# Optimization experiments

Measured on AMD Instinct MI355X. Metric: run time of the kernel, lower is better.

Reference implementation:

```python
import jax, jax.numpy as jnp
import numpy as np

D = 1024
H = 16
HD = D // H
EPS = 1e-9


def setup_inputs() -> dict:
    key = jax.random.key(0)
    ks = jax.random.split(key, 16)
    B, Lq, Lk = 8, 512, 1024
    s = 0.02
    return {
        "q": jax.random.normal(ks[0], (B, Lq, D), jnp.float32),
        "q_mask": jnp.ones((B, Lq), jnp.bool_),
        "kv": jax.random.normal(ks[1], (B, Lk, D), jnp.float32),
        "kv_mask": jnp.ones((B, Lk), jnp.bool_),
        # MultiheadAttention packed in-proj + out-proj
        "in_proj_w": jax.random.normal(ks[2], (3 * D, D), jnp.float32) * s,
        "in_proj_b": jnp.zeros((3 * D,), jnp.float32),
        "out_w": jax.random.normal(ks[3], (D, D), jnp.float32) * s,
        "out_b": jnp.zeros((D,), jnp.float32),
        # shared LayerNorm
        "ln_g": jnp.ones((D,), jnp.float32),
        "ln_b": jnp.zeros((D,), jnp.float32),
        # FFN
        "w1": jax.random.normal(ks[4], (4 * D, D), jnp.float32) * s,
        "b1": jnp.zeros((4 * D,), jnp.float32),
        "w2": jax.random.normal(ks[5], (D, 4 * D), jnp.float32) * s,
        "b2": jnp.zeros((D,), jnp.float32),
        # gate MLP
        "gw1": jax.random.normal(ks[6], (D, 2 * D), jnp.float32) * s,
        "gb1": jnp.zeros((D,), jnp.float32),
        "gw2": jax.random.normal(ks[7], (1, D), jnp.float32) * s,
        "gb2": jnp.zeros((1,), jnp.float32),
    }


def _layer_norm(x, g, b, eps=1e-5):
    mu = x.mean(-1, keepdims=True)
    var = ((x - mu) ** 2).mean(-1, keepdims=True)
    return (x - mu) * jax.lax.rsqrt(var + eps) * g + b


def reference(q, q_mask, kv, kv_mask, in_proj_w, in_proj_b, out_w, out_b,
              ln_g, ln_b, w1, b1, w2, b2, gw1, gb1, gw2, gb2):
    B, Lq, _ = q.shape
    Lk = kv.shape[1]
    # packed projections (torch Linear convention: x @ W.T + b)
    qp = (q @ in_proj_w[:D].T + in_proj_b[:D]).reshape(B, Lq, H, HD)
    kp = (kv @ in_proj_w[D:2 * D].T + in_proj_b[D:2 * D]).reshape(B, Lk, H, HD)
    vp = (kv @ in_proj_w[2 * D:].T + in_proj_b[2 * D:]).reshape(B, Lk, H, HD)
    scores = jnp.einsum('bqhd,bkhd->bhqk', qp, kp) / np.sqrt(HD)  # (B,H,Lq,Lk)
    scores = jnp.where(kv_mask[:, None, None, :], scores, -1e30)
    attn = jax.nn.softmax(scores, axis=-1)
    ctx = jnp.einsum('bhqk,bkhd->bqhd', attn, vp).reshape(B, Lq, D)
    attn_out = ctx @ out_w.T + out_b
    # entropy over keys, normalized by log(Lk), averaged over heads
    p = jnp.clip(attn, EPS)
    ent = -(p * jnp.log(p)).sum(-1) / jnp.log(jnp.float32(Lk))  # (B,H,Lq)
    ent = ent.mean(axis=1)[..., None]  # (B,Lq,1)
    conf = jnp.clip(1.0 - ent, 0.0, 1.0)
    # gate MLP on [q, attn_out]
    h = jax.nn.gelu(jnp.concatenate([q, attn_out], -1) @ gw1.T + gb1, approximate=False)
    g = jax.nn.sigmoid(h @ gw2.T + gb2) * conf
    q2 = _layer_norm(q + attn_out * g, ln_g, ln_b)
    ffn = jax.nn.gelu(q2 @ w1.T + b1, approximate=False) @ w2.T + b2
    q2 = _layer_norm(q2 + ffn, ln_g, ln_b)
    return q2, ent
```

## Files before the change

### kernel.cpp

```cpp
#include <hip/hip_runtime.h>
#include <cstdint>
#include <cstddef>

typedef __bf16 bf16;
typedef __bf16 bf16x8 __attribute__((ext_vector_type(8)));
typedef __bf16 bf16x4 __attribute__((ext_vector_type(4)));
typedef float  f32x4  __attribute__((ext_vector_type(4)));

#define GLOAD_LDS16(g, l) __builtin_amdgcn_global_load_lds( \
    (const __attribute__((address_space(1))) unsigned int*)(g), \
    (__attribute__((address_space(3))) unsigned int*)(l), 16, 0, 0)

static constexpr int D_  = 1024;
static constexpr int H_  = 16;
static constexpr int HD_ = 64;
static constexpr int B_  = 8;
static constexpr int LQ_ = 512;
static constexpr int LK_ = 1024;
static constexpr int MQ_ = B_ * LQ_;
static constexpr float LOG2E_ = 1.4426950408889634f;
static constexpr float INV_LN_LK_ = 0.14426950408889634f;
static constexpr float CSHIFT_ = 8.0f;

__device__ __forceinline__ float gelu_f(float v) {
    return 0.5f * v * (1.0f + erff(v * 0.70710678118654752f));
}

__global__ __launch_bounds__(256)
void cast_all_k(const float* __restrict__ ipw, const float* __restrict__ outw,
                const float* __restrict__ w1,  const float* __restrict__ w2,
                const float* __restrict__ gw1, const float* __restrict__ q,
                const float* __restrict__ kv,
                bf16* __restrict__ ipw_b, bf16* __restrict__ outw_b,
                bf16* __restrict__ w1_b,  bf16* __restrict__ w2_b,
                bf16* __restrict__ gw1_b, bf16* __restrict__ x_b,
                bf16* __restrict__ kv_b) {
    const int b = blockIdx.x, t = threadIdx.x;
    const float* src; bf16* dst; long e;
    if (b < 1536)       { src = ipw;  dst = ipw_b;  e = (long)b * 2048; }
    else if (b < 2048)  { src = outw; dst = outw_b; e = (long)(b - 1536) * 2048; }
    else if (b < 4096)  { src = w1;   dst = w1_b;   e = (long)(b - 2048) * 2048; }
    else if (b < 6144)  { src = w2;   dst = w2_b;   e = (long)(b - 4096) * 2048; }
    else if (b < 7168)  { src = gw1;  dst = gw1_b;  e = (long)(b - 6144) * 2048; }
    else if (b < 11264) { src = kv;   dst = kv_b;   e = (long)(b - 7168) * 2048; }
    else {
        long e2 = (long)(b - 11264) * 2048 + t * 8;
        float4 a = *(const float4*)(q + e2);
        float4 c = *(const float4*)(q + e2 + 4);
        bf16x8 o;
        o[0]=(bf16)a.x; o[1]=(bf16)a.y; o[2]=(bf16)a.z; o[3]=(bf16)a.w;
        o[4]=(bf16)c.x; o[5]=(bf16)c.y; o[6]=(bf16)c.z; o[7]=(bf16)c.w;
        long row = e2 >> 10, col = e2 & 1023;
        *(bf16x8*)(x_b + row * 2048 + col) = o;
        return;
    }
    e += t * 8;
    float4 a = *(const float4*)(src + e);
    float4 c = *(const float4*)(src + e + 4);
    bf16x8 o;
    o[0]=(bf16)a.x; o[1]=(bf16)a.y; o[2]=(bf16)a.z; o[3]=(bf16)a.w;
    o[4]=(bf16)c.x; o[5]=(bf16)c.y; o[6]=(bf16)c.z; o[7]=(bf16)c.w;
    *(bf16x8*)(dst + e) = o;
}

template<int ACT>
__device__ __forceinline__
void gemm256_body(const bf16* __restrict__ A, int lda,
                  const bf16* __restrict__ W, int ldw,
                  const float* __restrict__ bias,
                  bf16* __restrict__ Cb, int ldcb, int K) {
    __shared__ __attribute__((aligned(16))) bf16 As[2][256 * 64];
    __shared__ __attribute__((aligned(16))) bf16 Bs[2][256 * 64];
    const int gx = gridDim.x;
    const int nwg = gx * gridDim.y;
    const int flat = blockIdx.x + gx * blockIdx.y;
    const int swzb = (flat & 7) * (nwg >> 3) + (flat >> 3);
    const int by = swzb / gx, bx = swzb - by * gx;
    const int t = threadIdx.x;
    const int w = t >> 6, l = t & 63, l15 = l & 15, lg = l >> 4;
    const int wr = w >> 2, wc = w & 3;
    const int row0 = by * 256, col0 = bx * 256;
    const int sw = l15 & 7;

    size_t aoff[4], woff[4];
    int ldsoff[4];
#pragma unroll
    for (int j = 0; j < 4; ++j) {
        int id = j * 512 + t;
        int r = id >> 3, c = id & 7;
        aoff[j] = (size_t)(row0 + r) * lda + ((c ^ (r & 7)) << 3);
        woff[j] = (size_t)(col0 + r) * ldw + ((c ^ (r & 7)) << 3);
        ldsoff[j] = (j * 512 + w * 64) * 8;
    }

    f32x4 acc[8][4];
#pragma unroll
    for (int m = 0; m < 8; ++m)
#pragma unroll
        for (int n = 0; n < 4; ++n) acc[m][n] = f32x4{0.f, 0.f, 0.f, 0.f};

    const int nt = K >> 6;
#pragma unroll
    for (int j = 0; j < 4; ++j) {
        GLOAD_LDS16(A + aoff[j], (bf16*)As[0] + ldsoff[j]);
        GLOAD_LDS16(W + woff[j], (bf16*)Bs[0] + ldsoff[j]);
    }
    __syncthreads();

    for (int kt = 0; kt < nt; ++kt) {
        const int cur = kt & 1;
        if (kt + 1 < nt) {
            const size_t k0 = (size_t)(kt + 1) * 64;
            bf16* dA = (bf16*)As[cur ^ 1];
            bf16* dB = (bf16*)Bs[cur ^ 1];
#pragma unroll
            for (int j = 0; j < 4; ++j) {
                GLOAD_LDS16(A + aoff[j] + k0, dA + ldsoff[j]);
                GLOAD_LDS16(W + woff[j] + k0, dB + ldsoff[j]);
            }
        }
        const bf16* Ac = As[cur];
        const bf16* Bc = Bs[cur];
#pragma unroll
        for (int ks2 = 0; ks2 < 2; ++ks2) {
            bf16x8 af[8], bfr[4];
#pragma unroll
            for (int m = 0; m < 8; ++m) {
                int ra = wr * 128 + m * 16 + l15;
                af[m] = *(const bf16x8*)&Ac[ra * 64 + (((ks2 * 4 + lg) ^ sw) << 3)];
            }
#pragma unroll
            for (int n = 0; n < 4; ++n) {
                int rb = wc * 64 + n * 16 + l15;
                bfr[n] = *(const bf16x8*)&Bc[rb * 64 + (((ks2 * 4 + lg) ^ sw) << 3)];
            }
#pragma unroll
            for (int m = 0; m < 8; ++m)
#pragma unroll
                for (int n = 0; n < 4; ++n)
                    acc[m][n] = __builtin_amdgcn_mfma_f32_16x16x32_bf16(af[m], bfr[n], acc[m][n], 0, 0, 0);
        }
        __syncthreads();
    }

#pragma unroll
    for (int n = 0; n < 4; ++n) {
        int gcol = col0 + wc * 64 + n * 16 + l15;
        float bv = bias[gcol];
#pragma unroll
        for (int m = 0; m < 8; ++m) {
            int grow = row0 + wr * 128 + m * 16 + lg * 4;
#pragma unroll
            for (int r = 0; r < 4; ++r) {
                float v = acc[m][n][r] + bv;
                if (ACT) v = gelu_f(v);
                Cb[(size_t)(grow + r) * ldcb + gcol] = (bf16)v;
            }
        }
    }
}

__global__ __launch_bounds__(512, 2)
void gemm256_kvproj_k(const bf16* A, const bf16* W, const float* bias, bf16* Cb) {
    gemm256_body<0>(A, 1024, W, 1024, bias, Cb, 2048, 1024);
}
__global__ __launch_bounds__(512, 2)
void gemm256_ffn1_k(const bf16* A, const bf16* W, const float* bias, bf16* Cb) {
    gemm256_body<1>(A, 1024, W, 1024, bias, Cb, 4096, 1024);
}

template<int ACT, int OUTB, int OUTF>
__device__ __forceinline__
void gemm_body(const bf16* __restrict__ A, int lda,
               const bf16* __restrict__ W, int ldw,
               const float* __restrict__ bias,
               bf16* __restrict__ Cb, int ldcb,
               float* __restrict__ Cf, int ldcf,
               int K) {
    __shared__ __attribute__((aligned(16))) bf16 As[128 * 32];
    __shared__ __attribute__((aligned(16))) bf16 Bs[128 * 32];
    const int gx = gridDim.x;
    const int nwg = gx * gridDim.y;
    const int flat = blockIdx.x + gx * blockIdx.y;
    const int swz = (flat & 7) * (nwg >> 3) + (flat >> 3);
    const int by = swz / gx, bx = swz - by * gx;
    const int t = threadIdx.x;
    const int w = t >> 6, l = t & 63;
    const int l15 = l & 15, lg = l >> 4;
    const int row0 = by * 128, col0 = bx * 128;
    const int wr = (w >> 1) * 64, wc = (w & 1) * 64;

    f32x4 acc[4][4];
#pragma unroll
    for (int m = 0; m < 4; ++m)
#pragma unroll
        for (int n = 0; n < 4; ++n) acc[m][n] = f32x4{0.f, 0.f, 0.f, 0.f};

    const int nk = K >> 5;
    for (int ks = 0; ks < nk; ++ks) {
        __syncthreads();
        const int k0 = ks * 32;
#pragma unroll
        for (int i = 0; i < 2; ++i) {
            int f = i * 256 + t;
            int rr = f >> 2, c8 = (f & 3) * 8;
            GLOAD_LDS16(A + (size_t)(row0 + rr) * lda + k0 + c8,
                        As + (size_t)(i * 256 + w * 64) * 8);
            GLOAD_LDS16(W + (size_t)(col0 + rr) * ldw + k0 + c8,
                        Bs + (size_t)(i * 256 + w * 64) * 8);
        }
        __syncthreads();
        bf16x8 af[4], bfm[4];
#pragma unroll
        for (int m = 0; m < 4; ++m)
            af[m] = *(const bf16x8*)&As[(wr + m * 16 + l15) * 32 + lg * 8];
#pragma unroll
        for (int n = 0; n < 4; ++n)
            bfm[n] = *(const bf16x8*)&Bs[(wc + n * 16 + l15) * 32 + lg * 8];
#pragma unroll
        for (int m = 0; m < 4; ++m)
#pragma unroll
            for (int n = 0; n < 4; ++n)
                acc[m][n] = __builtin_amdgcn_mfma_f32_16x16x32_bf16(af[m], bfm[n], acc[m][n], 0, 0, 0);
    }

#pragma unroll
    for (int n = 0; n < 4; ++n) {
        int gcol = col0 + wc + n * 16 + l15;
        float bv = bias ? bias[gcol] : 0.f;
#pragma unroll
        for (int m = 0; m < 4; ++m) {
            int grow = row0 + wr + m * 16 + lg * 4;
#pragma unroll
            for (int r = 0; r < 4; ++r) {
                float v = acc[m][n][r] + bv;
                if (ACT == 1) v = gelu_f(v);
                if (OUTB) Cb[(size_t)(grow + r) * ldcb + gcol] = (bf16)v;
                if (OUTF) Cf[(size_t)(grow + r) * ldcf + gcol] = v;
            }
        }
    }
}

__device__ __forceinline__
void gemm_splitk_body(const bf16* __restrict__ A, int lda,
                      const bf16* __restrict__ W, int ldw,
                      float* __restrict__ C0, float* __restrict__ C1, int ldcf,
                      int K, int aoff, int woff) {
    __shared__ __attribute__((aligned(16))) bf16 As[128 * 32];
    __shared__ __attribute__((aligned(16))) bf16 Bs[128 * 32];
    const int gx = gridDim.x, gy = gridDim.y;
    const int nwg = gx * gy * gridDim.z;
    const int flat = blockIdx.x + gx * (blockIdx.y + gy * blockIdx.z);
    const int swz = (flat & 7) * (nwg >> 3) + (flat >> 3);
    const int z = swz / (gx * gy);
    const int rem = swz - z * (gx * gy);
    const int by = rem / gx, bx = rem - by * gx;
    A += (size_t)z * aoff;
    W += (size_t)z * woff;
    float* Cf = z ? C1 : C0;

    const int t = threadIdx.x;
    const int w = t >> 6, l = t & 63;
    const int l15 = l & 15, lg = l >> 4;
    const int row0 = by * 128, col0 = bx * 128;
    const int wr = (w >> 1) * 64, wc = (w & 1) * 64;

    f32x4 acc[4][4];
#pragma unroll
    for (int m = 0; m < 4; ++m)
#pragma unroll
        for (int n = 0; n < 4; ++n) acc[m][n] = f32x4{0.f, 0.f, 0.f, 0.f};

    const int nk = K >> 5;
    for (int ks = 0; ks < nk; ++ks) {
        __syncthreads();
        const int k0 = ks * 32;
#pragma unroll
        for (int i = 0; i < 2; ++i) {
            int f = i * 256 + t;
            int rr = f >> 2, c8 = (f & 3) * 8;
            GLOAD_LDS16(A + (size_t)(row0 + rr) * lda + k0 + c8,
                        As + (size_t)(i * 256 + w * 64) * 8);
            GLOAD_LDS16(W + (size_t)(col0 + rr) * ldw + k0 + c8,
                        Bs + (size_t)(i * 256 + w * 64) * 8);
        }
        __syncthreads();
        bf16x8 af[4], bfm[4];
#pragma unroll
        for (int m = 0; m < 4; ++m)
            af[m] = *(const bf16x8*)&As[(wr + m * 16 + l15) * 32 + lg * 8];
#pragma unroll
        for (int n = 0; n < 4; ++n)
            bfm[n] = *(const bf16x8*)&Bs[(wc + n * 16 + l15) * 32 + lg * 8];
#pragma unroll
        for (int m = 0; m < 4; ++m)
#pragma unroll
            for (int n = 0; n < 4; ++n)
                acc[m][n] = __builtin_amdgcn_mfma_f32_16x16x32_bf16(af[m], bfm[n], acc[m][n], 0, 0, 0);
    }

#pragma unroll
    for (int n = 0; n < 4; ++n) {
        int gcol = col0 + wc + n * 16 + l15;
#pragma unroll
        for (int m = 0; m < 4; ++m) {
            int grow = row0 + wr + m * 16 + lg * 4;
#pragma unroll
            for (int r = 0; r < 4; ++r)
                Cf[(size_t)(grow + r) * ldcf + gcol] = acc[m][n][r];
        }
    }
}

__global__ __launch_bounds__(256)
void gemm_qproj_k(const bf16* A, const bf16* W, const float* bias, bf16* Cb) {
    gemm_body<0,1,0>(A, 2048, W, 1024, bias, Cb, 1024, nullptr, 0, 1024);
}
__global__ __launch_bounds__(256)
void gemm_outproj_k(const bf16* A, const bf16* W, const float* bias, bf16* Cb) {
    gemm_body<0,1,0>(A, 1024, W, 1024, bias, Cb, 2048, nullptr, 0, 1024);
}
__global__ __launch_bounds__(256)
void gemm_gate2_k(const bf16* A, const bf16* W, float* C0, float* C1) {
    gemm_splitk_body(A, 2048, W, 2048, C0, C1, 1024, 1024, 1024, 1024);
}
__global__ __launch_bounds__(256)
void gemm_ffn2_k(const bf16* A, const bf16* W, float* C0, float* C1) {
    gemm_splitk_body(A, 4096, W, 4096, C0, C1, 1024, 2048, 2048, 2048);
}

__device__ __forceinline__ float red16sum(float v) {
    v += __shfl_xor(v, 1, 64);
    v += __shfl_xor(v, 2, 64);
    v += __shfl_xor(v, 4, 64);
    v += __shfl_xor(v, 8, 64);
    return v;
}

__global__ __launch_bounds__(256)
void attn_k(const bf16* __restrict__ Qp, const bf16* __restrict__ KVp,
            bf16* __restrict__ ctx, float* __restrict__ entm) {
    __shared__ __attribute__((aligned(16))) bf16 Ks[64 * 72];
    __shared__ __attribute__((aligned(16))) bf16 Vts[64 * 72];
    __shared__ __attribute__((aligned(16))) bf16 Ps[4][16 * 72];
    const int t = threadIdx.x, w = t >> 6, l = t & 63;
    const int l15 = l & 15, lg = l >> 4;
    const int h = blockIdx.x, b = blockIdx.y, qt = blockIdx.z;
    const int qrow0 = b * LQ_ + qt * 64 + w * 16;

    bf16x8 aq[2];
#pragma unroll
    for (int kk = 0; kk < 2; ++kk)
        aq[kk] = *(const bf16x8*)(Qp + (size_t)(qrow0 + l15) * D_ + h * HD_ + kk * 32 + lg * 8);

    f32x4 o[4];
    float Zp[4], S1p[4];
#pragma unroll
    for (int n = 0; n < 4; ++n) o[n] = f32x4{0.f, 0.f, 0.f, 0.f};
#pragma unroll
    for (int r = 0; r < 4; ++r) { Zp[r] = 0.f; S1p[r] = 0.f; }

    const float K1 = 0.125f * LOG2E_;
    const float K0 = -CSHIFT_ * LOG2E_;

    for (int c = 0; c < LK_ / 64; ++c) {
        __syncthreads();
        const int kbase = b * LK_ + c * 64;
#pragma unroll
        for (int i = 0; i < 2; ++i) {
            int f = i * 256 + t;
            int key = f >> 3, seg = f & 7;
            const bf16* kvrow = KVp + (size_t)(kbase + key) * 2048 + h * HD_ + seg * 8;
            bf16x8 k8 = *(const bf16x8*)kvrow;
            bf16x8 v8 = *(const bf16x8*)(kvrow + 1024);
            *(bf16x8*)&Ks[key * 72 + seg * 8] = k8;
            int vcol = key ^ (seg << 3);
#pragma unroll
            for (int j = 0; j < 8; ++j) Vts[(seg * 8 + j) * 72 + vcol] = v8[j];
        }
        __syncthreads();

        f32x4 s[4];
#pragma unroll
        for (int n = 0; n < 4; ++n) {
            s[n] = f32x4{0.f, 0.f, 0.f, 0.f};
#pragma unroll
            for (int kk = 0; kk < 2; ++kk) {
                bf16x8 bk = *(const bf16x8*)&Ks[(n * 16 + l15) * 72 + kk * 32 + lg * 8];
                s[n] = __builtin_amdgcn_mfma_f32_16x16x32_bf16(aq[kk], bk, s[n], 0, 0, 0);
            }
        }

        float p[4][4];
#pragma unroll
        for (int r = 0; r < 4; ++r) {
#pragma unroll
            for (int n = 0; n < 4; ++n) {
                float sv = s[n][r];
                float pv = exp2f(fmaf(sv, K1, K0));
                p[n][r] = pv;
                Zp[r] += pv;
                S1p[r] = fmaf(pv, sv, S1p[r]);
            }
        }

#pragma unroll
        for (int r = 0; r < 4; ++r)
#pragma unroll
            for (int n = 0; n < 4; ++n)
                Ps[w][(lg * 4 + r) * 72 + ((n ^ lg) << 4) + l15] = (bf16)p[n][r];

        bf16x8 ap[2];
#pragma unroll
        for (int kk = 0; kk < 2; ++kk)
            ap[kk] = *(const bf16x8*)&Ps[w][l15 * 72 + ((kk * 32 + lg * 8) ^ (((l15 >> 2) & 3) << 4))];
#pragma unroll
        for (int n = 0; n < 4; ++n) {
            const int segd = (n * 2 + (l15 >> 3)) & 7;
#pragma unroll
            for (int kk = 0; kk < 2; ++kk) {
                bf16x8 bv = *(const bf16x8*)&Vts[(n * 16 + l15) * 72 + (((kk * 4 + lg) ^ segd) << 3)];
                o[n] = __builtin_amdgcn_mfma_f32_16x16x32_bf16(ap[kk], bv, o[n], 0, 0, 0);
            }
        }
    }

#pragma unroll
    for (int r = 0; r < 4; ++r) {
        float Zr = red16sum(Zp[r]);
        float S1r = red16sum(S1p[r]) * 0.125f;
        float inv = 1.0f / Zr;
        int grow = qrow0 + lg * 4 + r;
#pragma unroll
        for (int n = 0; n < 4; ++n)
            ctx[(size_t)grow * D_ + h * HD_ + n * 16 + l15] = (bf16)(o[n][r] * inv);
        if (l15 == 0) {
            float ent = (CSHIFT_ + logf(Zr) - S1r * inv) * INV_LN_LK_ * (1.0f / 16.0f);
            atomicAdd(&entm[grow], ent);
        }
    }
}

__device__ __forceinline__ float blk_sum(float v, float* sb) {
#pragma unroll
    for (int m = 1; m < 64; m <<= 1) v += __shfl_xor(v, m, 64);
    int w = threadIdx.x >> 6;
    __syncthreads();
    if ((threadIdx.x & 63) == 0) sb[w] = v;
    __syncthreads();
    return sb[0] + sb[1] + sb[2] + sb[3];
}
__device__ __forceinline__ float2 blk_sum2(float2 v, float* sb) {
#pragma unroll
    for (int m = 1; m < 64; m <<= 1) {
        v.x += __shfl_xor(v.x, m, 64);
        v.y += __shfl_xor(v.y, m, 64);
    }
    int w = threadIdx.x >> 6;
    __syncthreads();
    if ((threadIdx.x & 63) == 0) { sb[w * 2] = v.x; sb[w * 2 + 1] = v.y; }
    __syncthreads();
    return make_float2(sb[0] + sb[2] + sb[4] + sb[6], sb[1] + sb[3] + sb[5] + sb[7]);
}

__global__ __launch_bounds__(256)
void gate_ln1_k(const float* __restrict__ qin, const bf16* __restrict__ xb,
                const float* __restrict__ gp0, const float* __restrict__ gp1,
                const float* __restrict__ gb1, const float* __restrict__ gw2,
                const float* __restrict__ gb2, const float* __restrict__ entm,
                const float* __restrict__ lng, const float* __restrict__ lnb,
                float* __restrict__ q2f, bf16* __restrict__ q2b) {
    __shared__ float sb[8];
    const int row = blockIdx.x, t = threadIdx.x, c0 = t * 4;
    float4 p0 = *(const float4*)(gp0 + (size_t)row * D_ + c0);
    float4 p1 = *(const float4*)(gp1 + (size_t)row * D_ + c0);
    float4 hb = *(const float4*)(gb1 + c0);
    float h0 = gelu_f(p0.x + p1.x + hb.x);
    float h1 = gelu_f(p0.y + p1.y + hb.y);
    float h2 = gelu_f(p0.z + p1.z + hb.z);
    float h3 = gelu_f(p0.w + p1.w + hb.w);
    float4 g4 = *(const float4*)(gw2 + c0);
    float dot = h0 * g4.x + h1 * g4.y + h2 * g4.z + h3 * g4.w;
    dot = blk_sum(dot, sb);
    float g = 1.0f / (1.0f + expf(-(dot + gb2[0])));
    float conf = fminf(fmaxf(1.0f - entm[row], 0.0f), 1.0f);
    g *= conf;
    float4 qv = *(const float4*)(qin + (size_t)row * D_ + c0);
    bf16x4 a4 = *(const bf16x4*)(xb + (size_t)row * 2048 + 1024 + c0);
    float y[4] = { qv.x + (float)a4[0] * g, qv.y + (float)a4[1] * g,
                   qv.z + (float)a4[2] * g, qv.w + (float)a4[3] * g };
    float2 ss = blk_sum2(make_float2(y[0] + y[1] + y[2] + y[3],
                                     y[0]*y[0] + y[1]*y[1] + y[2]*y[2] + y[3]*y[3]), sb);
    float mu = ss.x * (1.0f / D_);
    float var = ss.y * (1.0f / D_) - mu * mu;
    float rs = rsqrtf(var + 1e-5f);
    float4 gg = *(const float4*)(lng + c0);
    float4 bb = *(const float4*)(lnb + c0);
    float o0 = (y[0] - mu) * rs * gg.x + bb.x;
    float o1 = (y[1] - mu) * rs * gg.y + bb.y;
    float o2 = (y[2] - mu) * rs * gg.z + bb.z;
    float o3 = (y[3] - mu) * rs * gg.w + bb.w;
    *(float4*)(q2f + (size_t)row * D_ + c0) = make_float4(o0, o1, o2, o3);
    bf16x4 ob; ob[0] = (bf16)o0; ob[1] = (bf16)o1; ob[2] = (bf16)o2; ob[3] = (bf16)o3;
    *(bf16x4*)(q2b + (size_t)row * D_ + c0) = ob;
}

__global__ __launch_bounds__(256)
void ln2_k(const float* __restrict__ q2f, const float* __restrict__ fp0,
           const float* __restrict__ fp1, const float* __restrict__ b2,
           const float* __restrict__ lng, const float* __restrict__ lnb,
           float* __restrict__ outp) {
    __shared__ float sb[8];
    const int row = blockIdx.x, t = threadIdx.x, c0 = t * 4;
    float4 a = *(const float4*)(q2f + (size_t)row * D_ + c0);
    float4 f0 = *(const float4*)(fp0 + (size_t)row * D_ + c0);
    float4 f1 = *(const float4*)(fp1 + (size_t)row * D_ + c0);
    float4 bv = *(const float4*)(b2 + c0);
    float y[4] = { a.x + f0.x + f1.x + bv.x, a.y + f0.y + f1.y + bv.y,
                   a.z + f0.z + f1.z + bv.z, a.w + f0.w + f1.w + bv.w };
    float2 ss = blk_sum2(make_float2(y[0] + y[1] + y[2] + y[3],
                                     y[0]*y[0] + y[1]*y[1] + y[2]*y[2] + y[3]*y[3]), sb);
    float mu = ss.x * (1.0f / D_);
    float var = ss.y * (1.0f / D_) - mu * mu;
    float rs = rsqrtf(var + 1e-5f);
    float4 gg = *(const float4*)(lng + c0);
    float4 bb = *(const float4*)(lnb + c0);
    *(float4*)(outp + (size_t)row * D_ + c0) = make_float4(
        (y[0] - mu) * rs * gg.x + bb.x, (y[1] - mu) * rs * gg.y + bb.y,
        (y[2] - mu) * rs * gg.z + bb.z, (y[3] - mu) * rs * gg.w + bb.w);
}

extern "C" void kernel_launch(void* const* d_in, const int* in_sizes, int n_in,
                              void* d_out, int out_size, void* d_ws, size_t ws_size,
                              hipStream_t stream) {
    (void)in_sizes; (void)n_in; (void)out_size; (void)ws_size;
    const float* q    = (const float*)d_in[0];
    const float* kv   = (const float*)d_in[2];
    const float* ipw  = (const float*)d_in[4];
    const float* ipb  = (const float*)d_in[5];
    const float* outw = (const float*)d_in[6];
    const float* outb = (const float*)d_in[7];
    const float* lng  = (const float*)d_in[8];
    const float* lnb  = (const float*)d_in[9];
    const float* w1   = (const float*)d_in[10];
    const float* b1   = (const float*)d_in[11];
    const float* w2   = (const float*)d_in[12];
    const float* b2   = (const float*)d_in[13];
    const float* gw1  = (const float*)d_in[14];
    const float* gb1  = (const float*)d_in[15];
    const float* gw2  = (const float*)d_in[16];
    const float* gb2  = (const float*)d_in[17];

    char* ws = (char*)d_ws;
    const size_t MB = 1u << 20;
    bf16*  ipw_b  = (bf16*)(ws + 0);
    bf16*  outw_b = (bf16*)(ws + 6 * MB);
    bf16*  w1_b   = (bf16*)(ws + 8 * MB);
    bf16*  w2_b   = (bf16*)(ws + 16 * MB);
    bf16*  gw1_b  = (bf16*)(ws + 24 * MB);
    bf16*  x_b    = (bf16*)(ws + 28 * MB);
    bf16*  kv_b   = (bf16*)(ws + 44 * MB);
    bf16*  Qp     = (bf16*)(ws + 60 * MB);
    bf16*  KVp    = (bf16*)(ws + 68 * MB);
    bf16*  ctx    = (bf16*)(ws + 100 * MB);
    float* gp0    = (float*)(ws + 44 * MB);
    float* gp1    = (float*)(ws + 60 * MB);
    float* q2f    = (float*)(ws + 76 * MB);
    bf16*  q2b    = (bf16*)(ws + 100 * MB);
    bf16*  h1     = (bf16*)(ws + 44 * MB);
    float* fp0    = (float*)(ws + 28 * MB);
    float* fp1    = (float*)(ws + 0);

    float* out  = (float*)d_out;
    float* entm = out + (size_t)MQ_ * D_;

    (void)hipMemsetAsync(entm, 0, (size_t)MQ_ * sizeof(float), stream);

    cast_all_k<<<13312, 256, 0, stream>>>(ipw, outw, w1, w2, gw1, q, kv,
                                          ipw_b, outw_b, w1_b, w2_b, gw1_b, x_b, kv_b);

    gemm_qproj_k<<<dim3(8, 32), 256, 0, stream>>>(x_b, ipw_b, ipb, Qp);
    gemm256_kvproj_k<<<dim3(8, 32), 512, 0, stream>>>(kv_b, ipw_b + 1024 * 1024, ipb + 1024, KVp);
    attn_k<<<dim3(H_, B_, LQ_ / 64), 256, 0, stream>>>(Qp, KVp, ctx, entm);
    gemm_outproj_k<<<dim3(8, 32), 256, 0, stream>>>(ctx, outw_b, outb, x_b + 1024);
    gemm_gate2_k<<<dim3(8, 32, 2), 256, 0, stream>>>(x_b, gw1_b, gp0, gp1);
    gate_ln1_k<<<MQ_, 256, 0, stream>>>(q, x_b, gp0, gp1, gb1, gw2, gb2, entm, lng, lnb, q2f, q2b);
    gemm256_ffn1_k<<<dim3(16, 16), 512, 0, stream>>>(q2b, w1_b, b1, h1);
    gemm_ffn2_k<<<dim3(8, 32, 2), 256, 0, stream>>>(h1, w2_b, fp0, fp1);
    ln2_k<<<MQ_, 256, 0, stream>>>(q2f, fp0, fp1, b2, lng, lnb, out);
}
```

Measured before the change: 314.9 us.

## Restructure 256x256 GEMM with half-tile staging, deeper prefetch and LDS-staged epilogue

The 256-tile GEMM used by the KV projection and FFN1 now loads each K-step as two 128-row half-tiles into a four-slot LDS ring. Loads are issued two steps ahead, with explicit vmcnt waits and raw barriers replacing __syncthreads, and MFMA runs under raised wave priority (s_setprio). The block swizzle is changed to group blocks into 8x4 regions. The epilogue stages results through LDS so each wave writes 16-byte vectorized global stores instead of scattered 2-byte stores. This targets memory latency stalls and uncoalesced output writes, at the cost of more barriers and a hard-coded grid shape assumption in the swizzle.

After: 324.2 us. +3.0%, slower.

```diff
diff --git a/kernel.cpp b/kernel.cpp
--- a/kernel.cpp
+++ b/kernel.cpp
@@ -65,33 +65,40 @@
 
 template<int ACT>
 __device__ __forceinline__
-void gemm256_body(const bf16* __restrict__ A, int lda,
-                  const bf16* __restrict__ W, int ldw,
-                  const float* __restrict__ bias,
-                  bf16* __restrict__ Cb, int ldcb, int K) {
-    __shared__ __attribute__((aligned(16))) bf16 As[2][256 * 64];
-    __shared__ __attribute__((aligned(16))) bf16 Bs[2][256 * 64];
+void gemm256p_body(const bf16* __restrict__ A, int lda,
+                   const bf16* __restrict__ W, int ldw,
+                   const float* __restrict__ bias,
+                   bf16* __restrict__ Cb, int ldcb, int K) {
+    __shared__ __attribute__((aligned(16))) bf16 LA[4 * 128 * 64];
+    __shared__ __attribute__((aligned(16))) bf16 LB[4 * 128 * 64];
     const int gx = gridDim.x;
-    const int nwg = gx * gridDim.y;
     const int flat = blockIdx.x + gx * blockIdx.y;
-    const int swzb = (flat & 7) * (nwg >> 3) + (flat >> 3);
-    const int by = swzb / gx, bx = swzb - by * gx;
+    const int nrx = gx >> 2;
+    const int xc = flat & 7, ii = flat >> 3;
+    const int ry = xc / nrx, rx = xc - ry * nrx;
+    const int by = ry * 8 + (ii >> 2), bx = rx * 4 + (ii & 3);
     const int t = threadIdx.x;
     const int w = t >> 6, l = t & 63, l15 = l & 15, lg = l >> 4;
     const int wr = w >> 2, wc = w & 3;
     const int row0 = by * 256, col0 = bx * 256;
     const int sw = l15 & 7;
 
-    size_t aoff[4], woff[4];
-    int ldsoff[4];
-#pragma unroll
-    for (int j = 0; j < 4; ++j) {
-        int id = j * 512 + t;
-        int r = id >> 3, c = id & 7;
-        aoff[j] = (size_t)(row0 + r) * lda + ((c ^ (r & 7)) << 3);
-        woff[j] = (size_t)(col0 + r) * ldw + ((c ^ (r & 7)) << 3);
-        ldsoff[j] = (j * 512 + w * 64) * 8;
-    }
+    const int tr = t >> 3;
+    const int scol = ((t & 7) ^ (tr & 7)) << 3;
+    const bf16* pA = A + (size_t)(row0 + tr) * lda + scol;
+    const bf16* pB = W + (size_t)(col0 + tr) * ldw + scol;
+    const int ldso = w * 512;
+
+    auto STAGE_UNIT = [&](int kt, int h) {
+        const int s = ((kt & 1) << 1) | h;
+        const size_t kc = (size_t)kt * 64;
+        const size_t ro = (size_t)h * 128;
+#pragma unroll
+        for (int j = 0; j < 2; ++j) {
+            GLOAD_LDS16(pA + (ro + j * 64) * lda + kc, (bf16*)LA + s * 8192 + j * 4096 + ldso);
+            GLOAD_LDS16(pB + (ro + j * 64) * ldw + kc, (bf16*)LB + s * 8192 + j * 4096 + ldso);
+        }
+    };
 
     f32x4 acc[8][4];
 #pragma unroll
@@ -100,73 +107,77 @@
         for (int n = 0; n < 4; ++n) acc[m][n] = f32x4{0.f, 0.f, 0.f, 0.f};
 
     const int nt = K >> 6;
-#pragma unroll
-    for (int j = 0; j < 4; ++j) {
-        GLOAD_LDS16(A + aoff[j], (bf16*)As[0] + ldsoff[j]);
-        GLOAD_LDS16(W + woff[j], (bf16*)Bs[0] + ldsoff[j]);
-    }
-    __syncthreads();
+    STAGE_UNIT(0, 0); STAGE_UNIT(0, 1); STAGE_UNIT(1, 0); STAGE_UNIT(1, 1);
+    asm volatile("s_waitcnt vmcnt(8)" ::: "memory");
+    __builtin_amdgcn_s_barrier();
 
     for (int kt = 0; kt < nt; ++kt) {
-        const int cur = kt & 1;
-        if (kt + 1 < nt) {
-            const size_t k0 = (size_t)(kt + 1) * 64;
-            bf16* dA = (bf16*)As[cur ^ 1];
-            bf16* dB = (bf16*)Bs[cur ^ 1];
-#pragma unroll
-            for (int j = 0; j < 4; ++j) {
-                GLOAD_LDS16(A + aoff[j] + k0, dA + ldsoff[j]);
-                GLOAD_LDS16(W + woff[j] + k0, dB + ldsoff[j]);
-            }
-        }
-        const bf16* Ac = As[cur];
-        const bf16* Bc = Bs[cur];
+        const bf16* Au = (const bf16*)LA + ((((kt & 1) << 1) | wr) * 8192);
+        const bf16* Bu = (const bf16*)LB + ((((kt & 1) << 1) | (wc >> 1)) * 8192);
+        const int rb = (wc & 1) << 6;
 #pragma unroll
         for (int ks2 = 0; ks2 < 2; ++ks2) {
             bf16x8 af[8], bfr[4];
-#pragma unroll
-            for (int m = 0; m < 8; ++m) {
-                int ra = wr * 128 + m * 16 + l15;
-                af[m] = *(const bf16x8*)&Ac[ra * 64 + (((ks2 * 4 + lg) ^ sw) << 3)];
-            }
-#pragma unroll
-            for (int n = 0; n < 4; ++n) {
-                int rb = wc * 64 + n * 16 + l15;
-                bfr[n] = *(const bf16x8*)&Bc[rb * 64 + (((ks2 * 4 + lg) ^ sw) << 3)];
-            }
+            const int kcol = ((ks2 * 4 + lg) ^ sw) << 3;
+#pragma unroll
+            for (int m = 0; m < 8; ++m)
+                af[m] = *(const bf16x8*)&Au[(m * 16 + l15) * 64 + kcol];
+#pragma unroll
+            for (int n = 0; n < 4; ++n)
+                bfr[n] = *(const bf16x8*)&Bu[(rb + n * 16 + l15) * 64 + kcol];
+            __builtin_amdgcn_s_barrier();
+            __builtin_amdgcn_s_setprio(1);
 #pragma unroll
             for (int m = 0; m < 8; ++m)
 #pragma unroll
                 for (int n = 0; n < 4; ++n)
                     acc[m][n] = __builtin_amdgcn_mfma_f32_16x16x32_bf16(af[m], bfr[n], acc[m][n], 0, 0, 0);
-        }
-        __syncthreads();
-    }
-
-#pragma unroll
-    for (int n = 0; n < 4; ++n) {
-        int gcol = col0 + wc * 64 + n * 16 + l15;
-        float bv = bias[gcol];
-#pragma unroll
-        for (int m = 0; m < 8; ++m) {
-            int grow = row0 + wr * 128 + m * 16 + lg * 4;
+            __builtin_amdgcn_s_setprio(0);
+            __builtin_amdgcn_s_barrier();
+        }
+        if (kt + 2 < nt) {
+            STAGE_UNIT(kt + 2, 0);
+            STAGE_UNIT(kt + 2, 1);
+            asm volatile("s_waitcnt vmcnt(8)" ::: "memory");
+        } else {
+            asm volatile("s_waitcnt vmcnt(0)" ::: "memory");
+        }
+        __builtin_amdgcn_s_barrier();
+    }
+
+    float bvn[4];
+#pragma unroll
+    for (int n = 0; n < 4; ++n) bvn[n] = bias[col0 + wc * 64 + n * 16 + l15];
+    const int erow = l >> 2, ec = (l & 3) * 16;
+#pragma unroll
+    for (int m = 0; m < 8; ++m) {
+        bf16* ep = (bf16*)LA + ((m & 1) * 8 + w) * 1152;
+#pragma unroll
+        for (int n = 0; n < 4; ++n)
 #pragma unroll
             for (int r = 0; r < 4; ++r) {
-                float v = acc[m][n][r] + bv;
+                float v = acc[m][n][r] + bvn[n];
                 if (ACT) v = gelu_f(v);
-                Cb[(size_t)(grow + r) * ldcb + gcol] = (bf16)v;
+                ep[(lg * 4 + r) * 72 + n * 16 + l15] = (bf16)v;
             }
-        }
+        asm volatile("s_waitcnt lgkmcnt(0)" ::: "memory");
+        __builtin_amdgcn_sched_barrier(0);
+        bf16x8 v8a = *(const bf16x8*)&ep[erow * 72 + ec];
+        bf16x8 v8b = *(const bf16x8*)&ep[erow * 72 + ec + 8];
+        const int grow = row0 + wr * 128 + m * 16 + erow;
+        bf16* dst = Cb + (size_t)grow * ldcb + col0 + wc * 64 + ec;
+        *(bf16x8*)dst = v8a;
+        *(bf16x8*)(dst + 8) = v8b;
     }
 }
 
 __global__ __launch_bounds__(512, 2)
 void gemm256_kvproj_k(const bf16* A, const bf16* W, const float* bias, bf16* Cb) {
-    gemm256_body<0>(A, 1024, W, 1024, bias, Cb, 2048, 1024);
+    gemm256p_body<0>(A, 1024, W, 1024, bias, Cb, 2048, 1024);
 }
 __global__ __launch_bounds__(512, 2)
 void gemm256_ffn1_k(const bf16* A, const bf16* W, const float* bias, bf16* Cb) {
-    gemm256_body<1>(A, 1024, W, 1024, bias, Cb, 4096, 1024);
+    gemm256p_body<1>(A, 1024, W, 1024, bias, Cb, 4096, 1024);
 }
 
 template<int ACT, int OUTB, int OUTF>
```
